# Kernel optimization log

Hardware: AMD Instinct MI355X
Metric: run time of the kernel (lower is better)

Reference implementation:

```python
import jax, jax.numpy as jnp
import numpy as np

HEADS = 8
DIM_HEAD = 32
HTK = 576
WTK = 576


def layernorm(x, g, b, eps=1e-6):
    mu = x.mean(-1, keepdims=True)
    var = ((x - mu) ** 2).mean(-1, keepdims=True)
    return (x - mu) * jax.lax.rsqrt(var + eps) * g + b


def conv2d(x, w, b, pad, groups=1):
    y = jax.lax.conv_general_dilated(
        x, w, (1, 1), [(pad, pad), (pad, pad)],
        dimension_numbers=('NCHW', 'OIHW', 'NCHW'),
        feature_group_count=groups)
    return y + b[None, :, None, None]


def prune_attn(attn, htk, wtk):
    B, H, N, _ = attn.shape
    bi = jnp.arange(B)[:, None, None]
    hi = jnp.arange(H)[None, :, None]
    # row pruning: score rows by mean over keys, keep top-k rows
    row_scores = attn.mean(-1)                       # [B,H,N]
    _, top_row = jax.lax.top_k(row_scores, htk)      # [B,H,htk]
    row_mask = jnp.zeros((B, H, N), attn.dtype).at[bi, hi, top_row].set(1.0)
    # col pruning: score cols by mean over queries, keep top-k cols
    col_scores = attn.mean(-2)                       # [B,H,N]
    _, top_col = jax.lax.top_k(col_scores, wtk)
    col_mask = jnp.zeros((B, H, N), attn.dtype).at[bi, hi, top_col].set(1.0)
    return attn * row_mask[..., :, None] * col_mask[..., None, :]


def setup_inputs() -> dict:
    key = jax.random.key(0)
    ks = jax.random.split(key, 24)
    C = 256
    hid = C * 4
    g = C // 8
    s = 0.02
    inp = {
        'x': jax.random.normal(ks[0], (2, C, 48, 48), jnp.float32),
        'qkv_w': jax.random.normal(ks[1], (C, 3 * C), jnp.float32) * s,
        'out_w': jax.random.normal(ks[2], (C, C), jnp.float32) * s,
        'ln1_g': jnp.ones((C,), jnp.float32),
        'ln1_b': jnp.zeros((C,), jnp.float32),
        'ln2_g': jnp.ones((C,), jnp.float32),
        'ln2_b': jnp.zeros((C,), jnp.float32),
        'dw_w': jax.random.normal(ks[3], (C, 1, 3, 3), jnp.float32) * s,
        'dw_b': jnp.zeros((C,), jnp.float32),
        'pw_w': jax.random.normal(ks[4], (C, C, 1, 1), jnp.float32) * s,
        'pw_b': jnp.zeros((C,), jnp.float32),
        'sg1_w': jax.random.normal(ks[5], (g, C, 1, 1), jnp.float32) * s,
        'sg1_b': jnp.zeros((g,), jnp.float32),
        'sg2_w': jax.random.normal(ks[6], (1, g, 7, 7), jnp.float32) * s,
        'sg2_b': jnp.zeros((1,), jnp.float32),
        'cg1_w': jax.random.normal(ks[7], (g, C, 1, 1), jnp.float32) * s,
        'cg1_b': jnp.zeros((g,), jnp.float32),
        'cg2_w': jax.random.normal(ks[8], (C, g, 1, 1), jnp.float32) * s,
        'cg2_b': jnp.zeros((C,), jnp.float32),
        'ff_w1': jax.random.normal(ks[9], (C, hid), jnp.float32) * s,
        'ff_b1': jnp.zeros((hid,), jnp.float32),
        'ff_w2': jax.random.normal(ks[10], (hid, C), jnp.float32) * s,
        'ff_b2': jnp.zeros((C,), jnp.float32),
        'gamma1': jnp.full((1,), 0.5, jnp.float32),
        'gamma2': jnp.full((1,), 0.5, jnp.float32),
    }
    return inp


def reference(x, qkv_w, out_w, ln1_g, ln1_b, ln2_g, ln2_b, dw_w, dw_b,
              pw_w, pw_b, sg1_w, sg1_b, sg2_w, sg2_b, cg1_w, cg1_b,
              cg2_w, cg2_b, ff_w1, ff_b1, ff_w2, ff_b2, gamma1, gamma2):
    B, C, H, W = x.shape
    N = H * W
    # ---- dual-pruned self-attention branch ----
    xa = x.transpose(0, 2, 3, 1).reshape(B, N, C)
    xa = layernorm(xa, ln1_g, ln1_b)
    qkv = xa @ qkv_w                                    # [B,N,3C]
    q, k, v = jnp.split(qkv, 3, axis=-1)
    rs = lambda t: t.reshape(B, N, HEADS, DIM_HEAD).transpose(0, 2, 1, 3)
    q, k, v = rs(q), rs(k), rs(v)                       # [B,h,N,d]
    attn = jnp.einsum('bhid,bhjd->bhij', q, k) * (DIM_HEAD ** -0.5)
    attn = prune_attn(attn, HTK, WTK)
    attn = jax.nn.softmax(attn, axis=-1)
    o = jnp.einsum('bhij,bhjd->bhid', attn, v)
    o = o.transpose(0, 2, 1, 3).reshape(B, N, C) @ out_w
    x_attn = o.reshape(B, H, W, C).transpose(0, 3, 1, 2)
    # ---- conv branch ----
    xc = conv2d(x, dw_w, dw_b, pad=1, groups=C)
    xc = conv2d(xc, pw_w, pw_b, pad=0)
    xs = x_attn + xc
    # ---- gates ----
    sg = jax.nn.silu(conv2d(xs, sg1_w, sg1_b, pad=0))
    sg = jax.nn.sigmoid(conv2d(sg, sg2_w, sg2_b, pad=3))   # [B,1,H,W]
    cg = xs.mean(axis=(2, 3), keepdims=True)                # [B,C,1,1]
    cg = jax.nn.silu(conv2d(cg, cg1_w, cg1_b, pad=0))
    cg = jax.nn.sigmoid(conv2d(cg, cg2_w, cg2_b, pad=0))
    x2 = x + gamma1[0] * (xs * sg * cg)
    # ---- FFN ----
    normed = layernorm(x2.transpose(0, 2, 3, 1), ln2_g, ln2_b)
    h = jax.nn.gelu(normed @ ff_w1 + ff_b1, approximate=False)
    ff = (h @ ff_w2 + ff_b2).transpose(0, 3, 1, 2)
    return x2 + gamma2[0] * ff
```

## Files before the change

### kernel.cpp

```cpp
#include <hip/hip_runtime.h>
#include <math.h>

#define N_PIX 2304
#define CCH   256
#define BHN   16
#define KTOP  576
#define NROWS 4608

typedef unsigned short u16;
typedef __attribute__((ext_vector_type(8))) short short8v;
typedef __attribute__((ext_vector_type(4))) float floatx4;

__device__ __forceinline__ u16 f2b(float f) {
  unsigned int u = __float_as_uint(f);
  return (u16)((u + 0x7fffu + ((u >> 16) & 1u)) >> 16);
}
__device__ __forceinline__ float b2f(u16 v) {
  return __uint_as_float(((unsigned int)v) << 16);
}

__device__ __forceinline__ void async16(const void* g, void* l) {
  __builtin_amdgcn_global_load_lds(
      (const __attribute__((address_space(1))) unsigned int*)g,
      (__attribute__((address_space(3))) unsigned int*)l, 16, 0, 0);
}

__device__ __forceinline__ float erf_apx(float x) {
  float ax = fabsf(x);
  float u = 1.f / (1.f + 0.3275911f * ax);
  float y = u * (0.254829592f + u * (-0.284496736f + u * (1.421413741f +
            u * (-1.453152027f + u * 1.061405429f))));
  float r = 1.f - y * expf(-ax * ax);
  return (x < 0.f) ? -r : r;
}

__global__ __launch_bounds__(256) void lncast_kernel(
    const float* __restrict__ x, u16* __restrict__ xa_bf, float* __restrict__ xnhwc,
    const float* __restrict__ g, const float* __restrict__ beta,
    const float* __restrict__ qkv_w, const float* __restrict__ out_w,
    const float* __restrict__ pw_w, const float* __restrict__ ff_w1,
    const float* __restrict__ ff_w2, const float* __restrict__ sg1_w,
    u16* __restrict__ qkvBT, u16* __restrict__ B2,
    u16* __restrict__ ff1BT, u16* __restrict__ ff2BT, u16* __restrict__ sg1BT,
    float* __restrict__ zbuf)
{
  __shared__ float tile[32 * 257];
  __shared__ float redS[8 * 32], redQ[8 * 32];
  __shared__ float mu_s[32], rs_s[32];
  int tid = threadIdx.x;
  if (blockIdx.x == 3536) {
#pragma unroll
    for (int j = 0; j < 10; ++j) zbuf[tid + j * 256] = 0.f;
    return;
  }
  if (blockIdx.x >= 144) {
    int i = (blockIdx.x - 144) * 256 + tid;
    if (i < 196608) { int k = i / 768, n = i - k * 768; qkvBT[n * 256 + k] = f2b(qkv_w[i]); return; }
    i -= 196608;
    if (i < 65536) { int k = i >> 8, n = i & 255; B2[n * 512 + k] = f2b(out_w[i]); return; }
    i -= 65536;
    if (i < 65536) { int n = i >> 8, ic = i & 255; B2[n * 512 + 256 + ic] = f2b(pw_w[i]); return; }
    i -= 65536;
    if (i < 262144) { int k = i >> 10, n = i & 1023; ff1BT[n * 256 + k] = f2b(ff_w1[i]); return; }
    i -= 262144;
    if (i < 262144) { int k = i & 1023, n = i >> 10; ff2BT[i] = f2b(ff_w2[k * 256 + n]); return; }
    i -= 262144;
    if (i < 16384) sg1BT[i] = (i < 8192) ? f2b(sg1_w[i]) : (u16)0;
    return;
  }
  int p0g = blockIdx.x * 32;
  int bb = p0g / N_PIX; int p0 = p0g - bb * N_PIX;
  int px = tid & 31, csub = tid >> 5;
  float sacc = 0.f, qacc = 0.f;
#pragma unroll 4
  for (int it = 0; it < 32; ++it) {
    int c = it * 8 + csub;
    float v = x[((long)bb * 256 + c) * N_PIX + p0 + px];
    tile[px * 257 + c] = v;
    sacc += v; qacc += v * v;
  }
  redS[csub * 32 + px] = sacc; redQ[csub * 32 + px] = qacc;
  __syncthreads();
  if (tid < 32) {
    float s = 0.f, qq = 0.f;
#pragma unroll
    for (int j = 0; j < 8; ++j) { s += redS[j * 32 + tid]; qq += redQ[j * 32 + tid]; }
    float mu = s * (1.f / 256.f);
    float var = qq * (1.f / 256.f) - mu * mu;
    mu_s[tid] = mu; rs_s[tid] = rsqrtf(var + 1e-6f);
  }
  __syncthreads();
  float gv = g[tid], bv = beta[tid];
#pragma unroll 4
  for (int it = 0; it < 32; ++it) {
    float v = tile[it * 257 + tid];
    long orow = (long)(p0g + it) * 256 + tid;
    xnhwc[orow] = v;
    xa_bf[orow] = f2b((v - mu_s[it]) * rs_s[it] * gv + bv);
  }
}

template<int MT, int EPI, int CS>
__global__ __launch_bounds__(256) void mgemm(
    const u16* __restrict__ A, const u16* __restrict__ BT,
    float* __restrict__ C, u16* __restrict__ C2,
    int K, int ldc, int nvalid,
    const float* __restrict__ bias, const float* __restrict__ add,
    const float* __restrict__ gamma,
    float* __restrict__ cs_out, int cs_ld,
    const u16* __restrict__ xs2, const float* __restrict__ sgv,
    const float* __restrict__ cgv, const float* __restrict__ g1p)
{
  __shared__ u16 Als[MT * 64 * 32];
  __shared__ u16 Bls[64 * 32];
  int tid = threadIdx.x;
  int w = tid >> 6, lane = tid & 63;
  int row0 = blockIdx.y * (MT * 64), col0 = blockIdx.x * 64;
  const u16* Abase = A + (long)row0 * K;
  const u16* Bbase = BT + (long)col0 * K;
  int q = lane >> 4, l15 = lane & 15;

  floatx4 acc[MT][4];
#pragma unroll
  for (int mi = 0; mi < MT; ++mi)
#pragma unroll
    for (int ni = 0; ni < 4; ++ni) acc[mi][ni] = (floatx4)0.f;

  int ccB = w * 64 + lane;
  int rB = ccB >> 2, kB = (ccB & 3) << 3;

  for (int k0 = 0; k0 < K; k0 += 32) {
#pragma unroll
    for (int i = 0; i < MT; ++i) {
      int cc = w * (64 * MT) + i * 64 + lane;
      async16(Abase + (long)(cc >> 2) * K + k0 + ((cc & 3) << 3), &Als[cc * 8]);
    }
    async16(Bbase + (long)rB * K + k0 + kB, &Bls[ccB * 8]);
    __syncthreads();
    short8v a[MT];
#pragma unroll
    for (int mi = 0; mi < MT; ++mi)
      a[mi] = *(const short8v*)&Als[(w * (16 * MT) + mi * 16 + l15) * 32 + q * 8];
#pragma unroll
    for (int ni = 0; ni < 4; ++ni) {
      short8v b = *(const short8v*)&Bls[(ni * 16 + l15) * 32 + q * 8];
#pragma unroll
      for (int mi = 0; mi < MT; ++mi)
        acc[mi][ni] = __builtin_amdgcn_mfma_f32_16x16x32_bf16(a[mi], b, acc[mi][ni], 0, 0, 0);
    }
    __syncthreads();
  }

  float g2 = (EPI == 5) ? gamma[0] : 0.f;
  float g1v = (EPI == 5) ? g1p[0] : 0.f;
  float cp[4] = {0.f, 0.f, 0.f, 0.f};
#pragma unroll
  for (int mi = 0; mi < MT; ++mi) {
#pragma unroll
    for (int ni = 0; ni < 4; ++ni) {
      int c = col0 + ni * 16 + l15;
      int rbase = row0 + w * (16 * MT) + mi * 16 + q * 4;
#pragma unroll
      for (int reg = 0; reg < 4; ++reg) {
        long row = rbase + reg;
        float v = acc[mi][ni][reg];
        if (EPI == 0) {
          C[row * ldc + c] = v;
          if (CS) cp[ni] += v;
        } else if (EPI == 3) {
          if (c < nvalid) {
            float t = v + bias[c];
            C[row * (long)nvalid + c] = t / (1.f + expf(-t));
          }
        } else if (EPI == 4) {
          float t = v + bias[c];
          t = 0.5f * t * (1.f + erf_apx(t * 0.70710678f));
          C2[row * ldc + c] = f2b(t);
        } else if (EPI == 5) {
          int bb = (int)(row / N_PIX); int p = (int)(row - (long)bb * N_PIX);
          float xsv = b2f(xs2[row * 256 + c]);
          float x2v = add[row * 256 + c] + g1v * xsv * sgv[row] * cgv[bb * 256 + c];
          float t = x2v + g2 * (v + bias[c]);
          C[((long)bb * 256 + c) * N_PIX + p] = t;
        } else if (EPI == 7) {
          float t = v + bias[c];
          C2[row * ldc + c] = f2b(t);
          if (CS) cp[ni] += t;
        }
      }
    }
  }
  if (CS) {
    int bb = (row0 >= N_PIX) ? 1 : 0;
#pragma unroll
    for (int ni = 0; ni < 4; ++ni) {
      float r = cp[ni];
      r += __shfl_xor(r, 16);
      r += __shfl_xor(r, 32);
      if (lane < 16) atomicAdd(&cs_out[bb * cs_ld + col0 + ni * 16 + l15], r);
    }
  }
}

__global__ __launch_bounds__(256) void tkdw_kernel(
    const float* __restrict__ qkv, const float* __restrict__ csum, int* __restrict__ out_idx,
    const float* __restrict__ xnhwc, const float* __restrict__ dw_w,
    const float* __restrict__ dw_b, u16* __restrict__ A2)
{
  __shared__ unsigned int u[N_PIX];
  __shared__ unsigned int hist[256];
  __shared__ unsigned int wtmp[4];
  __shared__ unsigned int sh_selbin, sh_selS;
  __shared__ unsigned int cnt_eq[4], cnt_sel[4];
  __shared__ float svl[32];
  int tid = threadIdx.x;
  if (blockIdx.x >= 32) {
    int pix = blockIdx.x - 32;
    int b = pix / N_PIX; int p = pix - b * N_PIX;
    int y = p / 48, xx = p - y * 48;
    int c = tid;
    float acc = dw_b[c];
#pragma unroll
    for (int ky = 0; ky < 3; ++ky) {
      int yy = y + ky - 1; if (yy < 0 || yy >= 48) continue;
#pragma unroll
      for (int kx = 0; kx < 3; ++kx) {
        int xc = xx + kx - 1; if (xc < 0 || xc >= 48) continue;
        acc += dw_w[c * 9 + ky * 3 + kx] * xnhwc[((long)(b * N_PIX + yy * 48 + xc)) * 256 + c];
      }
    }
    A2[(long)pix * 512 + 256 + c] = f2b(acc);
    return;
  }
  int bh = blockIdx.x & 15, which = blockIdx.x >> 4;
  int b = bh >> 3, h = bh & 7;
  int* out = out_idx + (which * BHN + bh) * KTOP;
  int wave = tid >> 6, lane = tid & 63;
  unsigned long long ltmask = (1ull << lane) - 1ull;
  if (tid < 32) svl[tid] = csum[b * 768 + (which ? 0 : 256) + h * 32 + tid];
  __syncthreads();
  int off = (which ? 256 : 0) + h * 32;
  for (int i = tid; i < N_PIX; i += 256) {
    const float4* p4 = (const float4*)(qkv + ((long)(b * N_PIX + i)) * 768 + off);
    float sc = 0.f;
#pragma unroll
    for (int j = 0; j < 8; ++j) {
      float4 v = p4[j];
      sc += v.x * svl[j * 4] + v.y * svl[j * 4 + 1] + v.z * svl[j * 4 + 2] + v.w * svl[j * 4 + 3];
    }
    unsigned int bu = __float_as_uint(sc);
    u[i] = (bu & 0x80000000u) ? ~bu : (bu | 0x80000000u);
  }
  __syncthreads();
  unsigned int prefix = 0u, kRem = KTOP;
  for (int pass = 0; pass < 4; ++pass) {
    int shift = 24 - pass * 8;
    hist[tid] = 0u;
    __syncthreads();
    unsigned int mask = (pass == 0) ? 0u : (0xFFFFFFFFu << (shift + 8));
    for (int i = tid; i < N_PIX; i += 256) {
      unsigned int v = u[i];
      if ((v & mask) == prefix) atomicAdd(&hist[(v >> shift) & 255u], 1u);
    }
    __syncthreads();
    int v = (int)hist[255 - tid];
    int xsc = v;
#pragma unroll
    for (int o = 1; o < 64; o <<= 1) { int y = __shfl_up(xsc, o); if (lane >= o) xsc += y; }
    if (lane == 63) wtmp[wave] = (unsigned int)xsc;
    __syncthreads();
    int wadd = 0;
    for (int ww = 0; ww < wave; ++ww) wadd += (int)wtmp[ww];
    unsigned int S = (unsigned int)(xsc + wadd - v);
    if (S < kRem && S + (unsigned int)v >= kRem) { sh_selbin = (unsigned int)(255 - tid); sh_selS = S; }
    __syncthreads();
    prefix |= (sh_selbin << shift);
    kRem -= sh_selS;
    __syncthreads();
  }
  unsigned int T = prefix;
  unsigned int run_sel = 0u, run_eq = 0u;
  for (int c0 = 0; c0 < N_PIX; c0 += 256) {
    int i = c0 + tid;
    unsigned int v = u[i];
    bool isGt = v > T, isEq = (v == T);
    unsigned long long be = __ballot(isEq);
    unsigned int eqpre = (unsigned int)__popcll(be & ltmask);
    if (lane == 0) cnt_eq[wave] = (unsigned int)__popcll(be);
    __syncthreads();
    unsigned int eqoff = run_eq + eqpre;
    for (int ww = 0; ww < wave; ++ww) eqoff += cnt_eq[ww];
    bool selF = isGt || (isEq && eqoff < kRem);
    unsigned long long bs = __ballot(selF);
    unsigned int spre = (unsigned int)__popcll(bs & ltmask);
    if (lane == 0) cnt_sel[wave] = (unsigned int)__popcll(bs);
    __syncthreads();
    unsigned int soff = run_sel + spre;
    for (int ww = 0; ww < wave; ++ww) soff += cnt_sel[ww];
    if (selF) out[soff] = i;
    unsigned int te = 0, ts = 0;
#pragma unroll
    for (int ww = 0; ww < 4; ++ww) { te += cnt_eq[ww]; ts += cnt_sel[ww]; }
    run_eq += te; run_sel += ts;
    __syncthreads();
  }
}

__global__ __launch_bounds__(256) void gather_kernel(
    const float* __restrict__ qkv, const int* __restrict__ idx,
    u16* __restrict__ Qg, u16* __restrict__ Kg, u16* __restrict__ VgT,
    float* __restrict__ vneg, const float* __restrict__ csum, u16* __restrict__ A2)
{
  __shared__ float red[256];
  int bh = blockIdx.y;
  int tid = threadIdx.x;
  int r = blockIdx.x * 8 + (tid >> 5);
  int d = tid & 31;
  int b = bh >> 3, h = bh & 7;
  int rn = idx[bh * KTOP + r];
  int cn = idx[(BHN + bh) * KTOP + r];
  const float scale = 0.17677669529663687f;
  float vv = qkv[((long)(b * N_PIX + cn)) * 768 + 512 + h * 32 + d];
  Qg [((long)bh * KTOP + r) * 32 + d] = f2b(qkv[((long)(b * N_PIX + rn)) * 768 + h * 32 + d] * scale);
  Kg [((long)bh * KTOP + r) * 32 + d] = f2b(qkv[((long)(b * N_PIX + cn)) * 768 + 256 + h * 32 + d]);
  VgT[((long)bh * 32 + d) * 584 + r] = f2b(vv);
  red[tid] = vv;
  int bid = blockIdx.y * 72 + blockIdx.x;
  int row = 4 * bid + (tid >> 6);
  int b2 = row / N_PIX;
  int c4 = (tid & 63) * 4;
  const float* vm = csum + b2 * 768 + 512 + c4;
  ushort4 ov;
  ov.x = f2b(vm[0] * (1.f / (float)N_PIX));
  ov.y = f2b(vm[1] * (1.f / (float)N_PIX));
  ov.z = f2b(vm[2] * (1.f / (float)N_PIX));
  ov.w = f2b(vm[3] * (1.f / (float)N_PIX));
  *(ushort4*)&A2[(long)row * 512 + c4] = ov;
  __syncthreads();
  if (tid < 32) {
    float s = 0.f;
#pragma unroll
    for (int j = 0; j < 8; ++j) s += red[j * 32 + tid];
    atomicAdd(&vneg[bh * 32 + tid], s);
  }
}

__global__ __launch_bounds__(256) void attn_kernel(
    const u16* __restrict__ Qg, const u16* __restrict__ Kg, const u16* __restrict__ VgT,
    const float* __restrict__ csum, const float* __restrict__ vneg,
    const int* __restrict__ idx, u16* __restrict__ A2)
{
  __shared__ u16 Pls[32 * 584];
  __shared__ float wmax[4 * 32], wsum[4 * 32];
  __shared__ float emv_s[32], invd_s[32], vdif_s[32];
  int bh = blockIdx.y;
  int row0 = blockIdx.x * 32;
  int tid = threadIdx.x;
  int w = tid >> 6, lane = tid & 63;
  int q = lane >> 4, l15 = lane & 15;
  int b = bh >> 3, h = bh & 7;
  if (tid < 32) vdif_s[tid] = csum[b * 768 + 512 + h * 32 + tid] - vneg[bh * 32 + tid];
  const u16* Qb = Qg + (long)bh * KTOP * 32;
  const u16* Kb = Kg + (long)bh * KTOP * 32;
  short8v af[2];
#pragma unroll
  for (int mi = 0; mi < 2; ++mi)
    af[mi] = *(const short8v*)(Qb + ((long)(row0 + mi * 16 + l15)) * 32 + q * 8);
  floatx4 sacc[2][9];
#pragma unroll
  for (int mi = 0; mi < 2; ++mi)
#pragma unroll
    for (int ni = 0; ni < 9; ++ni) sacc[mi][ni] = (floatx4)0.f;
#pragma unroll
  for (int ni = 0; ni < 9; ++ni) {
    int n = w * 144 + ni * 16 + l15;
    short8v bf = *(const short8v*)(Kb + (long)n * 32 + q * 8);
#pragma unroll
    for (int mi = 0; mi < 2; ++mi)
      sacc[mi][ni] = __builtin_amdgcn_mfma_f32_16x16x32_bf16(af[mi], bf, sacc[mi][ni], 0, 0, 0);
  }
#pragma unroll
  for (int mi = 0; mi < 2; ++mi)
#pragma unroll
    for (int reg = 0; reg < 4; ++reg) {
      float m = sacc[mi][0][reg];
#pragma unroll
      for (int ni = 1; ni < 9; ++ni) m = fmaxf(m, sacc[mi][ni][reg]);
#pragma unroll
      for (int o = 1; o < 16; o <<= 1) m = fmaxf(m, __shfl_xor(m, o));
      if (l15 == 0) wmax[w * 32 + mi * 16 + q * 4 + reg] = m;
    }
  __syncthreads();
#pragma unroll
  for (int mi = 0; mi < 2; ++mi)
#pragma unroll
    for (int reg = 0; reg < 4; ++reg) {
      int r = mi * 16 + q * 4 + reg;
      float gm = fmaxf(fmaxf(fmaxf(wmax[r], wmax[32 + r]), fmaxf(wmax[64 + r], wmax[96 + r])), 0.f);
      float s = 0.f;
#pragma unroll
      for (int ni = 0; ni < 9; ++ni) {
        float e = expf(sacc[mi][ni][reg] - gm);
        s += e;
        Pls[r * 584 + w * 144 + ni * 16 + l15] = f2b(e);
      }
#pragma unroll
      for (int o = 1; o < 16; o <<= 1) s += __shfl_xor(s, o);
      if (l15 == 0) wsum[w * 32 + r] = s;
    }
  __syncthreads();
  if (tid < 32) {
    float gm = fmaxf(fmaxf(fmaxf(wmax[tid], wmax[32 + tid]), fmaxf(wmax[64 + tid], wmax[96 + tid])), 0.f);
    float s = wsum[tid] + wsum[32 + tid] + wsum[64 + tid] + wsum[96 + tid];
    float em = expf(-gm);
    float inv = 1.f / (s + (float)(N_PIX - KTOP) * em);
    invd_s[tid] = inv;
    emv_s[tid] = em * inv;
  }
  __syncthreads();
  int mw = w & 1, nw = w >> 1;
  const u16* Vb = VgT + (long)bh * 32 * 584;
  floatx4 acc = (floatx4)0.f;
#pragma unroll
  for (int kt = 0; kt < 18; ++kt) {
    int k0 = kt * 32;
    short8v a = *(const short8v*)&Pls[(mw * 16 + l15) * 584 + k0 + q * 8];
    short8v bb = *(const short8v*)(Vb + (long)(nw * 16 + l15) * 584 + k0 + q * 8);
    acc = __builtin_amdgcn_mfma_f32_16x16x32_bf16(a, bb, acc, 0, 0, 0);
  }
  int d = nw * 16 + l15;
  float vd = vdif_s[d];
#pragma unroll
  for (int reg = 0; reg < 4; ++reg) {
    int r = mw * 16 + q * 4 + reg;
    float o = acc[reg] * invd_s[r] + emv_s[r] * vd;
    int n = idx[bh * KTOP + row0 + r];
    A2[((long)(b * N_PIX + n)) * 512 + h * 32 + d] = f2b(o);
  }
}

__global__ __launch_bounds__(256) void sgcg_kernel(
    const float* __restrict__ sga, const float* __restrict__ w,
    const float* __restrict__ b1, float* __restrict__ sgate,
    const float* __restrict__ cgm, const float* __restrict__ cw1, const float* __restrict__ cb1,
    const float* __restrict__ cw2, const float* __restrict__ cb2, float* __restrict__ cgate)
{
  __shared__ float ws[32 * 49];
  __shared__ float red[4 * 64];
  __shared__ float m[256];
  __shared__ float a[32];
  int t = threadIdx.x;
  if (blockIdx.x >= 96) {
    int b = blockIdx.x - 96;
    m[t] = cgm[b * 256 + t] * (1.f / (float)N_PIX);
    __syncthreads();
    if (t < 32) {
      float s = cb1[t];
      for (int c = 0; c < 256; ++c) s += cw1[t * 256 + c] * m[c];
      a[t] = s / (1.f + expf(-s));
    }
    __syncthreads();
    float s = cb2[t];
#pragma unroll
    for (int g = 0; g < 32; ++g) s += cw2[t * 32 + g] * a[g];
    cgate[b * 256 + t] = 1.f / (1.f + expf(-s));
    return;
  }
  int by = blockIdx.x; int b = by / 48, y = by - b * 48;
  for (int i = t; i < 32 * 49; i += 256) ws[i] = w[i];
  __syncthreads();
  int xx = t & 63, gg = t >> 6;
  float acc = 0.f;
  if (xx < 48) {
    for (int ky = 0; ky < 7; ++ky) {
      int yy = y + ky - 3; if (yy < 0 || yy >= 48) continue;
      for (int kx = 0; kx < 7; ++kx) {
        int xc = xx + kx - 3; if (xc < 0 || xc >= 48) continue;
        const float4* sp = (const float4*)(sga + ((long)(b * N_PIX + yy * 48 + xc)) * 32 + gg * 8);
        float4 v0 = sp[0], v1 = sp[1];
        int wb = gg * 8 * 49 + ky * 7 + kx;
        acc += ws[wb] * v0.x + ws[wb + 49] * v0.y + ws[wb + 98] * v0.z + ws[wb + 147] * v0.w;
        acc += ws[wb + 196] * v1.x + ws[wb + 245] * v1.y + ws[wb + 294] * v1.z + ws[wb + 343] * v1.w;
      }
    }
  }
  red[gg * 64 + xx] = acc;
  __syncthreads();
  if (t < 48) {
    float tot = b1[0] + red[t] + red[64 + t] + red[128 + t] + red[192 + t];
    sgate[b * N_PIX + y * 48 + t] = 1.f / (1.f + expf(-tot));
  }
}

__global__ __launch_bounds__(256) void gln_kernel(
    const float* __restrict__ xnhwc, const u16* __restrict__ xs_bf,
    const float* __restrict__ sgate, const float* __restrict__ cgate,
    const float* __restrict__ gamma1,
    const float* __restrict__ g, const float* __restrict__ bvec, u16* __restrict__ normed)
{
  __shared__ float red[256];
  int pix = blockIdx.x; int b = pix / N_PIX;
  int c = threadIdx.x;
  float xsv = b2f(xs_bf[(long)pix * 256 + c]);
  float v = xnhwc[(long)pix * 256 + c] + gamma1[0] * xsv * sgate[pix] * cgate[b * 256 + c];
  red[c] = v; __syncthreads();
  for (int off = 128; off > 0; off >>= 1) { if (c < off) red[c] += red[c + off]; __syncthreads(); }
  float mu = red[0] * (1.f / 256.f);
  __syncthreads();
  float dv = v - mu;
  red[c] = dv * dv; __syncthreads();
  for (int off = 128; off > 0; off >>= 1) { if (c < off) red[c] += red[c + off]; __syncthreads(); }
  float var = red[0] * (1.f / 256.f);
  normed[(long)pix * 256 + c] = f2b(dv * rsqrtf(var + 1e-6f) * g[c] + bvec[c]);
}

extern "C" void kernel_launch(void* const* d_in, const int* in_sizes, int n_in,
                              void* d_out, int out_size, void* d_ws, size_t ws_size,
                              hipStream_t stream) {
  (void)in_sizes; (void)n_in; (void)out_size; (void)ws_size;
  const float* x      = (const float*)d_in[0];
  const float* qkv_w  = (const float*)d_in[1];
  const float* out_w  = (const float*)d_in[2];
  const float* ln1_g  = (const float*)d_in[3];
  const float* ln1_b  = (const float*)d_in[4];
  const float* ln2_g  = (const float*)d_in[5];
  const float* ln2_b  = (const float*)d_in[6];
  const float* dw_w   = (const float*)d_in[7];
  const float* dw_b   = (const float*)d_in[8];
  const float* pw_w   = (const float*)d_in[9];
  const float* pw_b   = (const float*)d_in[10];
  const float* sg1_w  = (const float*)d_in[11];
  const float* sg1_b  = (const float*)d_in[12];
  const float* sg2_w  = (const float*)d_in[13];
  const float* sg2_b  = (const float*)d_in[14];
  const float* cg1_w  = (const float*)d_in[15];
  const float* cg1_b  = (const float*)d_in[16];
  const float* cg2_w  = (const float*)d_in[17];
  const float* cg2_b  = (const float*)d_in[18];
  const float* ff_w1  = (const float*)d_in[19];
  const float* ff_b1  = (const float*)d_in[20];
  const float* ff_w2  = (const float*)d_in[21];
  const float* ff_b2  = (const float*)d_in[22];
  const float* gamma1 = (const float*)d_in[23];
  const float* gamma2 = (const float*)d_in[24];
  float* out = (float*)d_out;
  float* ws  = (float*)d_ws;

  float* qkv     = ws + 0;
  u16*   A2      = (u16*)(ws + 3538944);
  float* xnhwc   = ws + 4718592;
  u16*   xa_bf   = (u16*)(ws + 5898240);
  u16*   xs_bf   = (u16*)(ws + 6488064);
  u16*   Qg_bf   = (u16*)(ws + 7077888);
  u16*   Kg_bf   = (u16*)(ws + 7225344);
  u16*   VgT     = (u16*)(ws + 7372800);
  float* sga     = ws + 7522304;
  float* csum    = ws + 7669760;
  float* vneg    = ws + 7671296;
  float* cgm     = ws + 7671808;
  float* sgate   = ws + 7672320;
  float* cgate   = ws + 7676928;
  int*   idxb    = (int*)(ws + 7677440);
  u16*   qkvBT   = (u16*)(ws + 7695872);
  u16*   B2combo = (u16*)(ws + 7794176);
  u16*   ff1BT   = (u16*)(ws + 7859712);
  u16*   ff2BT   = (u16*)(ws + 7990784);
  u16*   sg1BT   = (u16*)(ws + 8121856);
  u16*   h_bf     = (u16*)qkv;
  u16*   normed_bf= (u16*)(ws + 2359296);

  dim3 blk(256);

  lncast_kernel<<<dim3(3537), blk, 0, stream>>>(x, xa_bf, xnhwc, ln1_g, ln1_b,
      qkv_w, out_w, pw_w, ff_w1, ff_w2, sg1_w,
      qkvBT, B2combo, ff1BT, ff2BT, sg1BT, csum);

  mgemm<2, 0, 1><<<dim3(12, 36), blk, 0, stream>>>(xa_bf, qkvBT, qkv, nullptr,
      256, 768, 768, nullptr, nullptr, nullptr, csum, 768, nullptr, nullptr, nullptr, nullptr);
  tkdw_kernel<<<dim3(4640), blk, 0, stream>>>(qkv, csum, idxb, xnhwc, dw_w, dw_b, A2);
  gather_kernel<<<dim3(72, BHN), blk, 0, stream>>>(qkv, idxb, Qg_bf, Kg_bf, VgT, vneg,
      csum, A2);
  attn_kernel<<<dim3(18, BHN), blk, 0, stream>>>(Qg_bf, Kg_bf, VgT, csum, vneg, idxb, A2);

  mgemm<1, 7, 1><<<dim3(4, 72), blk, 0, stream>>>(A2, B2combo, nullptr, xs_bf,
      512, 256, 256, pw_b, nullptr, nullptr, cgm, 256, nullptr, nullptr, nullptr, nullptr);

  mgemm<1, 3, 0><<<dim3(1, 72), blk, 0, stream>>>(xs_bf, sg1BT, sga, nullptr,
      256, 32, 32, sg1_b, nullptr, nullptr, nullptr, 0, nullptr, nullptr, nullptr, nullptr);
  sgcg_kernel<<<dim3(98), blk, 0, stream>>>(sga, sg2_w, sg2_b, sgate,
      cgm, cg1_w, cg1_b, cg2_w, cg2_b, cgate);

  gln_kernel<<<dim3(NROWS), blk, 0, stream>>>(xnhwc, xs_bf, sgate, cgate, gamma1,
      ln2_g, ln2_b, normed_bf);

  mgemm<2, 4, 0><<<dim3(16, 36), blk, 0, stream>>>(normed_bf, ff1BT, nullptr, h_bf,
      256, 1024, 1024, ff_b1, nullptr, nullptr, nullptr, 0, nullptr, nullptr, nullptr, nullptr);
  mgemm<1, 5, 0><<<dim3(4, 72), blk, 0, stream>>>(h_bf, ff2BT, out, nullptr,
      1024, 256, 256, ff_b2, xnhwc, gamma2, nullptr, 0, xs_bf, sgate, cgate, gamma1);
}
```

Baseline: 248.3 us.

## Fold spatial-gate 1x1 conv into combined weights and store residual input as bf16

The sg1 1x1 conv is precomputed algebraically into the out/pw weight product (W3 = sg1_w·[out_w; pw_w], bias folded with pw_b). A new xsga kernel then computes xs and the gate pre-activations from A2 in one launch instead of two dependent GEMMs. Separately, the NHWC copy of x is stored as bf16 instead of fp32, halving its traffic in the depthwise conv, the gated layernorm and the final epilogue. The weight-folding GEMM runs as scalar loops inside lncast on every call, and bf16 residuals reduce accuracy of the skip path.

Result: no change. 253.0 us (+1.9%).

```diff
diff --git a/kernel.cpp b/kernel.cpp
--- a/kernel.cpp
+++ b/kernel.cpp
@@ -35,22 +35,45 @@
 }
 
 __global__ __launch_bounds__(256) void lncast_kernel(
-    const float* __restrict__ x, u16* __restrict__ xa_bf, float* __restrict__ xnhwc,
+    const float* __restrict__ x, u16* __restrict__ xa_bf, u16* __restrict__ xn_bf,
     const float* __restrict__ g, const float* __restrict__ beta,
     const float* __restrict__ qkv_w, const float* __restrict__ out_w,
     const float* __restrict__ pw_w, const float* __restrict__ ff_w1,
     const float* __restrict__ ff_w2, const float* __restrict__ sg1_w,
+    const float* __restrict__ sg1_b, const float* __restrict__ pw_b,
     u16* __restrict__ qkvBT, u16* __restrict__ B2,
-    u16* __restrict__ ff1BT, u16* __restrict__ ff2BT, u16* __restrict__ sg1BT,
-    float* __restrict__ zbuf)
+    u16* __restrict__ ff1BT, u16* __restrict__ ff2BT, u16* __restrict__ W3BT,
+    float* __restrict__ b3, float* __restrict__ zbuf)
 {
   __shared__ float tile[32 * 257];
   __shared__ float redS[8 * 32], redQ[8 * 32];
   __shared__ float mu_s[32], rs_s[32];
   int tid = threadIdx.x;
+  if (blockIdx.x == 3537) {
+#pragma unroll
+    for (int j = 0; j < 10; ++j) zbuf[tid + j * 256] = 0.f;
+    return;
+  }
   if (blockIdx.x == 3536) {
-#pragma unroll
-    for (int j = 0; j < 10; ++j) zbuf[tid + j * 256] = 0.f;
+    if (tid < 32) {
+      float s = sg1_b[tid];
+      for (int c = 0; c < 256; ++c) s += pw_b[c] * sg1_w[tid * 256 + c];
+      b3[tid] = s;
+    }
+    for (int j = tid; j < 16384; j += 256) W3BT[16384 + j] = 0;
+    return;
+  }
+  if (blockIdx.x >= 3472) {
+    int i = (blockIdx.x - 3472) * 256 + tid;
+    int gg = i >> 9, k = i & 511;
+    float s = 0.f;
+    if (k < 256) {
+      for (int c = 0; c < 256; ++c) s += sg1_w[gg * 256 + c] * out_w[k * 256 + c];
+    } else {
+      int ii = k - 256;
+      for (int c = 0; c < 256; ++c) s += sg1_w[gg * 256 + c] * pw_w[c * 256 + ii];
+    }
+    W3BT[gg * 512 + k] = f2b(s);
     return;
   }
   if (blockIdx.x >= 144) {
@@ -64,8 +87,6 @@
     if (i < 262144) { int k = i >> 10, n = i & 1023; ff1BT[n * 256 + k] = f2b(ff_w1[i]); return; }
     i -= 262144;
     if (i < 262144) { int k = i & 1023, n = i >> 10; ff2BT[i] = f2b(ff_w2[k * 256 + n]); return; }
-    i -= 262144;
-    if (i < 16384) sg1BT[i] = (i < 8192) ? f2b(sg1_w[i]) : (u16)0;
     return;
   }
   int p0g = blockIdx.x * 32;
@@ -95,7 +116,7 @@
   for (int it = 0; it < 32; ++it) {
     float v = tile[it * 257 + tid];
     long orow = (long)(p0g + it) * 256 + tid;
-    xnhwc[orow] = v;
+    xn_bf[orow] = f2b(v);
     xa_bf[orow] = f2b((v - mu_s[it]) * rs_s[it] * gv + bv);
   }
 }
@@ -104,8 +125,8 @@
 __global__ __launch_bounds__(256) void mgemm(
     const u16* __restrict__ A, const u16* __restrict__ BT,
     float* __restrict__ C, u16* __restrict__ C2,
-    int K, int ldc, int nvalid,
-    const float* __restrict__ bias, const float* __restrict__ add,
+    int K, int ldc,
+    const float* __restrict__ bias, const u16* __restrict__ addb,
     const float* __restrict__ gamma,
     float* __restrict__ cs_out, int cs_ld,
     const u16* __restrict__ xs2, const float* __restrict__ sgv,
@@ -167,11 +188,6 @@
         if (EPI == 0) {
           C[row * ldc + c] = v;
           if (CS) cp[ni] += v;
-        } else if (EPI == 3) {
-          if (c < nvalid) {
-            float t = v + bias[c];
-            C[row * (long)nvalid + c] = t / (1.f + expf(-t));
-          }
         } else if (EPI == 4) {
           float t = v + bias[c];
           t = 0.5f * t * (1.f + erf_apx(t * 0.70710678f));
@@ -179,13 +195,9 @@
         } else if (EPI == 5) {
           int bb = (int)(row / N_PIX); int p = (int)(row - (long)bb * N_PIX);
           float xsv = b2f(xs2[row * 256 + c]);
-          float x2v = add[row * 256 + c] + g1v * xsv * sgv[row] * cgv[bb * 256 + c];
+          float x2v = b2f(addb[row * 256 + c]) + g1v * xsv * sgv[row] * cgv[bb * 256 + c];
           float t = x2v + g2 * (v + bias[c]);
           C[((long)bb * 256 + c) * N_PIX + p] = t;
-        } else if (EPI == 7) {
-          float t = v + bias[c];
-          C2[row * ldc + c] = f2b(t);
-          if (CS) cp[ni] += t;
         }
       }
     }
@@ -202,9 +214,76 @@
   }
 }
 
+__global__ __launch_bounds__(256) void xsga_kernel(
+    const u16* __restrict__ A2, const u16* __restrict__ B2, const u16* __restrict__ W3BT,
+    u16* __restrict__ xs_bf, float* __restrict__ sga,
+    const float* __restrict__ pw_b, const float* __restrict__ b3,
+    float* __restrict__ cgm)
+{
+  __shared__ u16 Als[64 * 32];
+  __shared__ u16 Bls[64 * 32];
+  int tid = threadIdx.x;
+  int w = tid >> 6, lane = tid & 63;
+  int q = lane >> 4, l15 = lane & 15;
+  bool isSga = (blockIdx.x == 4);
+  int row0 = blockIdx.y * 64;
+  int col0 = isSga ? 0 : blockIdx.x * 64;
+  const u16* Abase = A2 + (long)row0 * 512;
+  const u16* Bbase = (isSga ? W3BT : B2) + (long)col0 * 512;
+
+  floatx4 acc[4];
+#pragma unroll
+  for (int ni = 0; ni < 4; ++ni) acc[ni] = (floatx4)0.f;
+  int cc = w * 64 + lane;
+  int rA = cc >> 2, kA = (cc & 3) << 3;
+
+  for (int k0 = 0; k0 < 512; k0 += 32) {
+    async16(Abase + (long)rA * 512 + k0 + kA, &Als[cc * 8]);
+    async16(Bbase + (long)rA * 512 + k0 + kA, &Bls[cc * 8]);
+    __syncthreads();
+    short8v a = *(const short8v*)&Als[(w * 16 + l15) * 32 + q * 8];
+#pragma unroll
+    for (int ni = 0; ni < 4; ++ni) {
+      short8v b = *(const short8v*)&Bls[(ni * 16 + l15) * 32 + q * 8];
+      acc[ni] = __builtin_amdgcn_mfma_f32_16x16x32_bf16(a, b, acc[ni], 0, 0, 0);
+    }
+    __syncthreads();
+  }
+
+  float cp[4] = {0.f, 0.f, 0.f, 0.f};
+#pragma unroll
+  for (int ni = 0; ni < 4; ++ni) {
+    int c = col0 + ni * 16 + l15;
+    int rbase = row0 + w * 16 + q * 4;
+#pragma unroll
+    for (int reg = 0; reg < 4; ++reg) {
+      long row = rbase + reg;
+      float v = acc[ni][reg];
+      if (!isSga) {
+        float t = v + pw_b[c];
+        xs_bf[row * 256 + c] = f2b(t);
+        cp[ni] += t;
+      } else if (c < 32) {
+        float t = v + b3[c];
+        sga[row * 32 + c] = t / (1.f + expf(-t));
+      }
+    }
+  }
+  if (!isSga) {
+    int bb = (row0 >= N_PIX) ? 1 : 0;
+#pragma unroll
+    for (int ni = 0; ni < 4; ++ni) {
+      float r = cp[ni];
+      r += __shfl_xor(r, 16);
+      r += __shfl_xor(r, 32);
+      if (lane < 16) atomicAdd(&cgm[bb * 256 + col0 + ni * 16 + l15], r);
+    }
+  }
+}
+
 __global__ __launch_bounds__(256) void tkdw_kernel(
     const float* __restrict__ qkv, const float* __restrict__ csum, int* __restrict__ out_idx,
-    const float* __restrict__ xnhwc, const float* __restrict__ dw_w,
+    const u16* __restrict__ xn_bf, const float* __restrict__ dw_w,
     const float* __restrict__ dw_b, u16* __restrict__ A2)
 {
   __shared__ unsigned int u[N_PIX];
@@ -226,7 +305,7 @@
 #pragma unroll
       for (int kx = 0; kx < 3; ++kx) {
         int xc = xx + kx - 1; if (xc < 0 || xc >= 48) continue;
-        acc += dw_w[c * 9 + ky * 3 + kx] * xnhwc[((long)(b * N_PIX + yy * 48 + xc)) * 256 + c];
+        acc += dw_w[c * 9 + ky * 3 + kx] * b2f(xn_bf[((long)(b * N_PIX + yy * 48 + xc)) * 256 + c]);
       }
     }
     A2[(long)pix * 512 + 256 + c] = f2b(acc);
@@ -493,7 +572,7 @@
 }
 
 __global__ __launch_bounds__(256) void gln_kernel(
-    const float* __restrict__ xnhwc, const u16* __restrict__ xs_bf,
+    const u16* __restrict__ xn_bf, const u16* __restrict__ xs_bf,
     const float* __restrict__ sgate, const float* __restrict__ cgate,
     const float* __restrict__ gamma1,
     const float* __restrict__ g, const float* __restrict__ bvec, u16* __restrict__ normed)
@@ -502,7 +581,7 @@
   int pix = blockIdx.x; int b = pix / N_PIX;
   int c = threadIdx.x;
   float xsv = b2f(xs_bf[(long)pix * 256 + c]);
-  float v = xnhwc[(long)pix * 256 + c] + gamma1[0] * xsv * sgate[pix] * cgate[b * 256 + c];
+  float v = b2f(xn_bf[(long)pix * 256 + c]) + gamma1[0] * xsv * sgate[pix] * cgate[b * 256 + c];
   red[c] = v; __syncthreads();
   for (int off = 128; off > 0; off >>= 1) { if (c < off) red[c] += red[c + off]; __syncthreads(); }
   float mu = red[0] * (1.f / 256.f);
@@ -548,53 +627,52 @@
 
   float* qkv     = ws + 0;
   u16*   A2      = (u16*)(ws + 3538944);
-  float* xnhwc   = ws + 4718592;
-  u16*   xa_bf   = (u16*)(ws + 5898240);
-  u16*   xs_bf   = (u16*)(ws + 6488064);
-  u16*   Qg_bf   = (u16*)(ws + 7077888);
-  u16*   Kg_bf   = (u16*)(ws + 7225344);
-  u16*   VgT     = (u16*)(ws + 7372800);
-  float* sga     = ws + 7522304;
-  float* csum    = ws + 7669760;
-  float* vneg    = ws + 7671296;
-  float* cgm     = ws + 7671808;
-  float* sgate   = ws + 7672320;
-  float* cgate   = ws + 7676928;
-  int*   idxb    = (int*)(ws + 7677440);
-  u16*   qkvBT   = (u16*)(ws + 7695872);
-  u16*   B2combo = (u16*)(ws + 7794176);
-  u16*   ff1BT   = (u16*)(ws + 7859712);
-  u16*   ff2BT   = (u16*)(ws + 7990784);
-  u16*   sg1BT   = (u16*)(ws + 8121856);
+  u16*   xn_bf   = (u16*)(ws + 4718592);
+  u16*   xa_bf   = (u16*)(ws + 5308416);
+  u16*   xs_bf   = (u16*)(ws + 5898240);
+  u16*   Qg_bf   = (u16*)(ws + 6488064);
+  u16*   Kg_bf   = (u16*)(ws + 6635520);
+  u16*   VgT     = (u16*)(ws + 6782976);
+  float* sga     = ws + 6932480;
+  float* csum    = ws + 7079936;
+  float* vneg    = ws + 7081472;
+  float* cgm     = ws + 7081984;
+  float* sgate   = ws + 7082496;
+  float* cgate   = ws + 7087104;
+  float* b3      = ws + 7087616;
+  int*   idxb    = (int*)(ws + 7087744);
+  u16*   qkvBT   = (u16*)(ws + 7106176);
+  u16*   B2combo = (u16*)(ws + 7204480);
+  u16*   ff1BT   = (u16*)(ws + 7270016);
+  u16*   ff2BT   = (u16*)(ws + 7401088);
+  u16*   W3BT    = (u16*)(ws + 7532160);
   u16*   h_bf     = (u16*)qkv;
   u16*   normed_bf= (u16*)(ws + 2359296);
 
   dim3 blk(256);
 
-  lncast_kernel<<<dim3(3537), blk, 0, stream>>>(x, xa_bf, xnhwc, ln1_g, ln1_b,
-      qkv_w, out_w, pw_w, ff_w1, ff_w2, sg1_w,
-      qkvBT, B2combo, ff1BT, ff2BT, sg1BT, csum);
+  lncast_kernel<<<dim3(3538), blk, 0, stream>>>(x, xa_bf, xn_bf, ln1_g, ln1_b,
+      qkv_w, out_w, pw_w, ff_w1, ff_w2, sg1_w, sg1_b, pw_b,
+      qkvBT, B2combo, ff1BT, ff2BT, W3BT, b3, csum);
 
   mgemm<2, 0, 1><<<dim3(12, 36), blk, 0, stream>>>(xa_bf, qkvBT, qkv, nullptr,
-      256, 768, 768, nullptr, nullptr, nullptr, csum, 768, nullptr, nullptr, nullptr, nullptr);
-  tkdw_kernel<<<dim3(4640), blk, 0, stream>>>(qkv, csum, idxb, xnhwc, dw_w, dw_b, A2);
+      256, 768, nullptr, nullptr, nullptr, csum, 768, nullptr, nullptr, nullptr, nullptr);
+  tkdw_kernel<<<dim3(4640), blk, 0, stream>>>(qkv, csum, idxb, xn_bf, dw_w, dw_b, A2);
   gather_kernel<<<dim3(72, BHN), blk, 0, stream>>>(qkv, idxb, Qg_bf, Kg_bf, VgT, vneg,
       csum, A2);
   attn_kernel<<<dim3(18, BHN), blk, 0, stream>>>(Qg_bf, Kg_bf, VgT, csum, vneg, idxb, A2);
 
-  mgemm<1, 7, 1><<<dim3(4, 72), blk, 0, stream>>>(A2, B2combo, nullptr, xs_bf,
-      512, 256, 256, pw_b, nullptr, nullptr, cgm, 256, nullptr, nullptr, nullptr, nullptr);
-
-  mgemm<1, 3, 0><<<dim3(1, 72), blk, 0, stream>>>(xs_bf, sg1BT, sga, nullptr,
-      256, 32, 32, sg1_b, nullptr, nullptr, nullptr, 0, nullptr, nullptr, nullptr, nullptr);
+  xsga_kernel<<<dim3(5, 72), blk, 0, stream>>>(A2, B2combo, W3BT, xs_bf, sga,
+      pw_b, b3, cgm);
+
   sgcg_kernel<<<dim3(98), blk, 0, stream>>>(sga, sg2_w, sg2_b, sgate,
       cgm, cg1_w, cg1_b, cg2_w, cg2_b, cgate);
 
-  gln_kernel<<<dim3(NROWS), blk, 0, stream>>>(xnhwc, xs_bf, sgate, cgate, gamma1,
+  gln_kernel<<<dim3(NROWS), blk, 0, stream>>>(xn_bf, xs_bf, sgate, cgate, gamma1,
       ln2_g, ln2_b, normed_bf);
 
   mgemm<2, 4, 0><<<dim3(16, 36), blk, 0, stream>>>(normed_bf, ff1BT, nullptr, h_bf,
-      256, 1024, 1024, ff_b1, nullptr, nullptr, nullptr, 0, nullptr, nullptr, nullptr, nullptr);
+      256, 1024, ff_b1, nullptr, nullptr, nullptr, 0, nullptr, nullptr, nullptr, nullptr);
   mgemm<1, 5, 0><<<dim3(4, 72), blk, 0, stream>>>(h_bf, ff2BT, out, nullptr,
-      1024, 256, 256, ff_b2, xnhwc, gamma2, nullptr, 0, xs_bf, sgate, cgate, gamma1);
-}
+      1024, 256, ff_b2, xn_bf, gamma2, nullptr, 0, xs_bf, sgate, cgate, gamma1);
+}
```
